# Kernel optimization log

Measured on AMD Instinct MI355X. Metric: run time of the kernel, lower is better.

## Reference

```python
import jax, jax.numpy as jnp
import numpy as np

NUM_HEADS = 16
D_ATT = 64


def setup_inputs() -> dict:
    key = jax.random.key(0)
    ks = jax.random.split(key, 7)
    b, n, hd = 4, 2048, NUM_HEADS * 64  # input last dim = num_heads * per-head embed_dim
    Q_vec = jax.random.normal(ks[0], (b, n, hd), dtype=jnp.float32)
    K_vec = jax.random.normal(ks[1], (b, n, hd), dtype=jnp.float32)
    V_vec = jax.random.normal(ks[2], (b, n, hd), dtype=jnp.float32)
    # torch Linear weights: [out_features, in_features] = [d_attention, per_head_dim]
    W_Q = jax.random.normal(ks[3], (D_ATT, 64), dtype=jnp.float32) * 0.02
    W_K = jax.random.normal(ks[4], (D_ATT, 64), dtype=jnp.float32) * 0.02
    W_V = jax.random.normal(ks[5], (D_ATT, 64), dtype=jnp.float32) * 0.02
    mask = jax.random.bernoulli(ks[6], p=0.9, shape=(b, n))  # bool [b, n]
    return {"Q_vec": Q_vec, "K_vec": K_vec, "V_vec": V_vec,
            "W_Q": W_Q, "W_K": W_K, "W_V": W_V, "mask": mask}


def reference(Q_vec, K_vec, V_vec, W_Q, W_K, W_V, mask):
    b, n, _ = Q_vec.shape
    h = NUM_HEADS
    scaling = 1.0 / np.sqrt(D_ATT).astype(np.float32)

    def split_heads(x):  # b n (h d) -> b h n d
        return x.reshape(b, n, h, -1).transpose(0, 2, 1, 3)

    # Linear applied per-head (weights are [out, in]; y = x @ W^T)
    q = split_heads(Q_vec) @ W_Q.T  # [b,h,n,D_ATT]
    k = split_heads(K_vec) @ W_K.T
    v = split_heads(V_vec) @ W_V.T

    dots = jnp.einsum('bhid,bhjd->bhij', q, k) * scaling  # [b,h,n,n]
    pair_mask = mask[:, None, :] & mask[:, :, None]       # [b,n,n]
    mask_value = -jnp.finfo(dots.dtype).max
    dots = jnp.where(pair_mask[:, None, :, :], dots, mask_value)
    attn = jax.nn.softmax(dots, axis=-1)
    out = jnp.einsum('bhij,bhjd->bhid', attn, v)          # [b,h,n,D_ATT]
    return out.transpose(0, 2, 1, 3).reshape(b, n, h * D_ATT)
```

## Files before the change

### kernel.cpp

```cpp
#include <hip/hip_runtime.h>

#define B_  4
#define N_  2048
#define H_  16
#define HD_ 1024

typedef short  bf16x8 __attribute__((ext_vector_type(8)));
typedef float  f32x4  __attribute__((ext_vector_type(4)));

static __device__ __forceinline__ unsigned short f2bf(float f) {
    unsigned int u = __builtin_bit_cast(unsigned int, f);
    u += 0x7FFFu + ((u >> 16) & 1u);
    return (unsigned short)(u >> 16);
}

__global__ __launch_bounds__(256) void proj_kernel(
    const float* __restrict__ Qv, const float* __restrict__ Kv,
    const float* __restrict__ Vv, const float* __restrict__ WQ,
    const float* __restrict__ WK, const float* __restrict__ WV,
    unsigned short* __restrict__ qs, unsigned short* __restrict__ ks,
    unsigned short* __restrict__ vt)
{
    __shared__ __align__(16) unsigned short xb[64][72];
    __shared__ __align__(16) unsigned short Wb[64][72];
    __shared__ __align__(16) unsigned short sb[64][72];

    const int tid  = threadIdx.x;
    const int wq   = tid >> 6;
    const int lane = tid & 63;
    const int l15  = lane & 15;
    const int quad = lane >> 4;

    const int i0 = blockIdx.x * 64;
    const int h  = blockIdx.y;
    const int b  = blockIdx.z;

    const size_t inbase = ((size_t)b * N_ + i0) * HD_ + h * 64;
    const size_t bh     = (size_t)b * H_ + h;

    #pragma unroll
    for (int p = 0; p < 3; ++p) {
        const float* W   = (p == 0) ? WQ : (p == 1) ? WK : WV;
        const float* inp = ((p == 0) ? Qv : (p == 1) ? Kv : Vv) + inbase;

        __syncthreads();
        for (int v = tid; v < 1024; v += 256) {
            int tok = v >> 4, c4 = (v & 15) * 4;
            float4 f = *reinterpret_cast<const float4*>(inp + (size_t)tok * HD_ + c4);
            uint2 u;
            u.x = f2bf(f.x) | ((unsigned)f2bf(f.y) << 16);
            u.y = f2bf(f.z) | ((unsigned)f2bf(f.w) << 16);
            *reinterpret_cast<uint2*>(&xb[tok][c4]) = u;
            float4 g = *reinterpret_cast<const float4*>(W + (size_t)v * 4);
            uint2 w2;
            w2.x = f2bf(g.x) | ((unsigned)f2bf(g.y) << 16);
            w2.y = f2bf(g.z) | ((unsigned)f2bf(g.w) << 16);
            *reinterpret_cast<uint2*>(&Wb[v >> 4][c4]) = w2;
        }
        __syncthreads();

        bf16x8 ax[2];
        #pragma unroll
        for (int kh = 0; kh < 2; ++kh)
            ax[kh] = *reinterpret_cast<const bf16x8*>(&xb[wq * 16 + l15][kh * 32 + quad * 8]);

        f32x4 C[4];
        #pragma unroll
        for (int t = 0; t < 4; ++t) {
            C[t] = f32x4{0.f, 0.f, 0.f, 0.f};
            #pragma unroll
            for (int kh = 0; kh < 2; ++kh) {
                bf16x8 bw = *reinterpret_cast<const bf16x8*>(&Wb[t * 16 + l15][kh * 32 + quad * 8]);
                C[t] = __builtin_amdgcn_mfma_f32_16x16x32_bf16(ax[kh], bw, C[t], 0, 0, 0);
            }
        }

        if (p < 2) {
            const float scl = (p == 0) ? 0.125f : 1.f;
            #pragma unroll
            for (int t = 0; t < 4; ++t)
                #pragma unroll
                for (int r = 0; r < 4; ++r)
                    sb[wq * 16 + quad * 4 + r][t * 16 + l15] = f2bf(C[t][r] * scl);
            __syncthreads();
            unsigned short* dst = ((p == 0) ? qs : ks) + ((size_t)bh * N_ + i0) * 64;
            for (int v = tid; v < 512; v += 256) {
                int row = v >> 3, c0 = (v & 7) * 8;
                *reinterpret_cast<uint4*>(dst + (size_t)row * 64 + c0) =
                    *reinterpret_cast<const uint4*>(&sb[row][c0]);
            }
        } else {
            #pragma unroll
            for (int t = 0; t < 4; ++t)
                #pragma unroll
                for (int r = 0; r < 4; ++r)
                    sb[t * 16 + l15][wq * 16 + quad * 4 + r] = f2bf(C[t][r]);
            __syncthreads();
            unsigned short* vdst = vt + (size_t)bh * 64 * N_ + i0;
            for (int v = tid; v < 512; v += 256) {
                int d = v >> 3, c0 = (v & 7) * 8;
                *reinterpret_cast<uint4*>(vdst + (size_t)d * N_ + c0) =
                    *reinterpret_cast<const uint4*>(&sb[d][c0]);
            }
        }
    }
}

__global__ __launch_bounds__(256) void attn_kernel(
    const unsigned short* __restrict__ qs, const unsigned short* __restrict__ ks,
    const unsigned short* __restrict__ vt, const int* __restrict__ maskp,
    float* __restrict__ out)
{
    __shared__ __align__(16) unsigned short Ks[64][72];
    __shared__ __align__(16) unsigned short Vt[64][72];
    __shared__ __align__(16) unsigned short Ps[4][16][72];
    __shared__ float kb[64];

    const int tid  = threadIdx.x;
    const int wq   = tid >> 6;
    const int lane = tid & 63;
    const int l15  = lane & 15;
    const int quad = lane >> 4;

    const int i0 = blockIdx.x * 64;
    const int bh = blockIdx.y;
    const int b  = bh >> 4;
    const int h  = bh & 15;

    const unsigned short* qrow = qs + ((size_t)bh * N_ + i0 + wq * 16 + l15) * 64;
    bf16x8 aq[2];
    aq[0] = *reinterpret_cast<const bf16x8*>(qrow + quad * 8);
    aq[1] = *reinterpret_cast<const bf16x8*>(qrow + 32 + quad * 8);

    float qm[4];
    #pragma unroll
    for (int r = 0; r < 4; ++r)
        qm[r] = maskp[b * N_ + i0 + wq * 16 + quad * 4 + r] ? 1.f : 0.f;

    bf16x8 bones;
    {
        short onev = (l15 == 0) ? (short)0x3F80 : (short)0;
        #pragma unroll
        for (int j = 0; j < 8; ++j) bones[j] = onev;
    }

    f32x4 O[4];
    f32x4 L = f32x4{0.f, 0.f, 0.f, 0.f};
    #pragma unroll
    for (int t = 0; t < 4; ++t) O[t] = f32x4{0.f, 0.f, 0.f, 0.f};

    const unsigned short* kbase = ks + (size_t)bh * N_ * 64;
    const unsigned short* vbase = vt + (size_t)bh * 64 * N_;

    for (int kv0 = 0; kv0 < N_; kv0 += 64) {
        __syncthreads();
        #pragma unroll
        for (int it = 0; it < 2; ++it) {
            int r  = (tid >> 3) + it * 32;
            int c0 = (tid & 7) * 8;
            *reinterpret_cast<uint4*>(&Ks[r][c0]) =
                *reinterpret_cast<const uint4*>(kbase + (size_t)(kv0 + r) * 64 + c0);
            *reinterpret_cast<uint4*>(&Vt[r][c0]) =
                *reinterpret_cast<const uint4*>(vbase + (size_t)r * N_ + kv0 + c0);
        }
        if (tid < 64) kb[tid] = maskp[b * N_ + kv0 + tid] ? 0.f : -1e30f;
        __syncthreads();

        f32x4 S[4];
        #pragma unroll
        for (int t = 0; t < 4; ++t) {
            S[t] = f32x4{0.f, 0.f, 0.f, 0.f};
            #pragma unroll
            for (int kh = 0; kh < 2; ++kh) {
                bf16x8 bk = *reinterpret_cast<const bf16x8*>(&Ks[t * 16 + l15][kh * 32 + quad * 8]);
                S[t] = __builtin_amdgcn_mfma_f32_16x16x32_bf16(aq[kh], bk, S[t], 0, 0, 0);
            }
        }

        float kbl[4];
        #pragma unroll
        for (int t = 0; t < 4; ++t) kbl[t] = kb[t * 16 + l15];

        #pragma unroll
        for (int t = 0; t < 4; ++t)
            #pragma unroll
            for (int r = 0; r < 4; ++r) {
                float s = (qm[r] != 0.f) ? (S[t][r] + kbl[t]) : 0.f;
                Ps[wq][quad * 4 + r][t * 16 + l15] = f2bf(__expf(s));
            }

        __builtin_amdgcn_s_waitcnt(0xC07F);

        bf16x8 ap[2];
        #pragma unroll
        for (int kh = 0; kh < 2; ++kh)
            ap[kh] = *reinterpret_cast<const bf16x8*>(&Ps[wq][l15][kh * 32 + quad * 8]);

        #pragma unroll
        for (int t = 0; t < 4; ++t) {
            #pragma unroll
            for (int kh = 0; kh < 2; ++kh) {
                bf16x8 bv = *reinterpret_cast<const bf16x8*>(&Vt[t * 16 + l15][kh * 32 + quad * 8]);
                O[t] = __builtin_amdgcn_mfma_f32_16x16x32_bf16(ap[kh], bv, O[t], 0, 0, 0);
            }
        }
        #pragma unroll
        for (int kh = 0; kh < 2; ++kh)
            L = __builtin_amdgcn_mfma_f32_16x16x32_bf16(ap[kh], bones, L, 0, 0, 0);
    }

    float invl[4];
    #pragma unroll
    for (int r = 0; r < 4; ++r) {
        float l = __shfl(L[r], lane & 48);
        invl[r] = 1.f / l;
    }
    #pragma unroll
    for (int t = 0; t < 4; ++t)
        #pragma unroll
        for (int r = 0; r < 4; ++r) {
            int i = i0 + wq * 16 + quad * 4 + r;
            out[((size_t)b * N_ + i) * HD_ + h * 64 + t * 16 + l15] = O[t][r] * invl[r];
        }
}

extern "C" void kernel_launch(void* const* d_in, const int* in_sizes, int n_in,
                              void* d_out, int out_size, void* d_ws, size_t ws_size,
                              hipStream_t stream)
{
    const float* Qv  = (const float*)d_in[0];
    const float* Kv  = (const float*)d_in[1];
    const float* Vv  = (const float*)d_in[2];
    const float* WQ  = (const float*)d_in[3];
    const float* WK  = (const float*)d_in[4];
    const float* WV  = (const float*)d_in[5];
    const int*   msk = (const int*)d_in[6];
    float* out = (float*)d_out;

    const size_t per = (size_t)B_ * H_ * N_ * 64;
    unsigned short* qsb = (unsigned short*)d_ws;
    unsigned short* ksb = qsb + per;
    unsigned short* vtb = ksb + per;

    proj_kernel<<<dim3(N_ / 64, H_, B_), 256, 0, stream>>>(Qv, Kv, Vv, WQ, WK, WV, qsb, ksb, vtb);
    attn_kernel<<<dim3(N_ / 64, B_ * H_), 256, 0, stream>>>(qsb, ksb, vtb, msk, out);
}
```

Baseline: 279.7 us.

## Split projection per Q/K/V block, fold log2e into exp2, swizzle K/V tile loads

The projection kernel now launches three times as many blocks, each handling one of Q, K or V rather than looping over all three. This raises parallelism and removes the barriers between the three passes. bf16 packing uses a byte-permute of two rounded values, and the V transpose write is vectorised. The attention kernel folds log2(e) into the Q scale so it can call exp2f, replaces the mask select with a multiply, and staggers the rows each thread loads for the K/V tiles to spread memory and LDS bank traffic.

```diff
diff --git a/kernel.cpp b/kernel.cpp
--- a/kernel.cpp
+++ b/kernel.cpp
@@ -12,6 +12,14 @@
     unsigned int u = __builtin_bit_cast(unsigned int, f);
     u += 0x7FFFu + ((u >> 16) & 1u);
     return (unsigned short)(u >> 16);
+}
+
+static __device__ __forceinline__ unsigned rne_hi(float f) {
+    unsigned u = __builtin_bit_cast(unsigned, f);
+    return u + 0x7FFFu + ((u >> 16) & 1u);
+}
+static __device__ __forceinline__ unsigned f2bf2pack(float lo, float hi) {
+    return __builtin_amdgcn_perm(rne_hi(hi), rne_hi(lo), 0x07060302u);
 }
 
 __global__ __launch_bounds__(256) void proj_kernel(
@@ -33,75 +41,75 @@
 
     const int i0 = blockIdx.x * 64;
     const int h  = blockIdx.y;
-    const int b  = blockIdx.z;
+    const int bz = blockIdx.z;
+    const int b  = bz / 3;
+    const int p  = bz - b * 3;
 
     const size_t inbase = ((size_t)b * N_ + i0) * HD_ + h * 64;
     const size_t bh     = (size_t)b * H_ + h;
 
-    #pragma unroll
-    for (int p = 0; p < 3; ++p) {
-        const float* W   = (p == 0) ? WQ : (p == 1) ? WK : WV;
-        const float* inp = ((p == 0) ? Qv : (p == 1) ? Kv : Vv) + inbase;
-
-        __syncthreads();
-        for (int v = tid; v < 1024; v += 256) {
-            int tok = v >> 4, c4 = (v & 15) * 4;
-            float4 f = *reinterpret_cast<const float4*>(inp + (size_t)tok * HD_ + c4);
+    const float* W   = (p == 0) ? WQ : (p == 1) ? WK : WV;
+    const float* inp = ((p == 0) ? Qv : (p == 1) ? Kv : Vv) + inbase;
+
+    for (int v = tid; v < 1024; v += 256) {
+        int tok = v >> 4, c4 = (v & 15) * 4;
+        float4 f = *reinterpret_cast<const float4*>(inp + (size_t)tok * HD_ + c4);
+        uint2 u;
+        u.x = f2bf2pack(f.x, f.y);
+        u.y = f2bf2pack(f.z, f.w);
+        *reinterpret_cast<uint2*>(&xb[tok][c4]) = u;
+        float4 g = *reinterpret_cast<const float4*>(W + (size_t)v * 4);
+        uint2 w2;
+        w2.x = f2bf2pack(g.x, g.y);
+        w2.y = f2bf2pack(g.z, g.w);
+        *reinterpret_cast<uint2*>(&Wb[tok][c4]) = w2;
+    }
+    __syncthreads();
+
+    bf16x8 ax[2];
+    #pragma unroll
+    for (int kh = 0; kh < 2; ++kh)
+        ax[kh] = *reinterpret_cast<const bf16x8*>(&xb[wq * 16 + l15][kh * 32 + quad * 8]);
+
+    f32x4 C[4];
+    #pragma unroll
+    for (int t = 0; t < 4; ++t) {
+        C[t] = f32x4{0.f, 0.f, 0.f, 0.f};
+        #pragma unroll
+        for (int kh = 0; kh < 2; ++kh) {
+            bf16x8 bw = *reinterpret_cast<const bf16x8*>(&Wb[t * 16 + l15][kh * 32 + quad * 8]);
+            C[t] = __builtin_amdgcn_mfma_f32_16x16x32_bf16(ax[kh], bw, C[t], 0, 0, 0);
+        }
+    }
+
+    if (p < 2) {
+        const float scl = (p == 0) ? 0.180336880f : 1.f;
+        #pragma unroll
+        for (int t = 0; t < 4; ++t)
+            #pragma unroll
+            for (int r = 0; r < 4; ++r)
+                sb[wq * 16 + quad * 4 + r][t * 16 + l15] = f2bf(C[t][r] * scl);
+        __syncthreads();
+        unsigned short* dst = ((p == 0) ? qs : ks) + ((size_t)bh * N_ + i0) * 64;
+        for (int v = tid; v < 512; v += 256) {
+            int row = v >> 3, c0 = (v & 7) * 8;
+            *reinterpret_cast<uint4*>(dst + (size_t)row * 64 + c0) =
+                *reinterpret_cast<const uint4*>(&sb[row][c0]);
+        }
+    } else {
+        #pragma unroll
+        for (int t = 0; t < 4; ++t) {
             uint2 u;
-            u.x = f2bf(f.x) | ((unsigned)f2bf(f.y) << 16);
-            u.y = f2bf(f.z) | ((unsigned)f2bf(f.w) << 16);
-            *reinterpret_cast<uint2*>(&xb[tok][c4]) = u;
-            float4 g = *reinterpret_cast<const float4*>(W + (size_t)v * 4);
-            uint2 w2;
-            w2.x = f2bf(g.x) | ((unsigned)f2bf(g.y) << 16);
-            w2.y = f2bf(g.z) | ((unsigned)f2bf(g.w) << 16);
-            *reinterpret_cast<uint2*>(&Wb[v >> 4][c4]) = w2;
-        }
-        __syncthreads();
-
-        bf16x8 ax[2];
-        #pragma unroll
-        for (int kh = 0; kh < 2; ++kh)
-            ax[kh] = *reinterpret_cast<const bf16x8*>(&xb[wq * 16 + l15][kh * 32 + quad * 8]);
-
-        f32x4 C[4];
-        #pragma unroll
-        for (int t = 0; t < 4; ++t) {
-            C[t] = f32x4{0.f, 0.f, 0.f, 0.f};
-            #pragma unroll
-            for (int kh = 0; kh < 2; ++kh) {
-                bf16x8 bw = *reinterpret_cast<const bf16x8*>(&Wb[t * 16 + l15][kh * 32 + quad * 8]);
-                C[t] = __builtin_amdgcn_mfma_f32_16x16x32_bf16(ax[kh], bw, C[t], 0, 0, 0);
-            }
-        }
-
-        if (p < 2) {
-            const float scl = (p == 0) ? 0.125f : 1.f;
-            #pragma unroll
-            for (int t = 0; t < 4; ++t)
-                #pragma unroll
-                for (int r = 0; r < 4; ++r)
-                    sb[wq * 16 + quad * 4 + r][t * 16 + l15] = f2bf(C[t][r] * scl);
-            __syncthreads();
-            unsigned short* dst = ((p == 0) ? qs : ks) + ((size_t)bh * N_ + i0) * 64;
-            for (int v = tid; v < 512; v += 256) {
-                int row = v >> 3, c0 = (v & 7) * 8;
-                *reinterpret_cast<uint4*>(dst + (size_t)row * 64 + c0) =
-                    *reinterpret_cast<const uint4*>(&sb[row][c0]);
-            }
-        } else {
-            #pragma unroll
-            for (int t = 0; t < 4; ++t)
-                #pragma unroll
-                for (int r = 0; r < 4; ++r)
-                    sb[t * 16 + l15][wq * 16 + quad * 4 + r] = f2bf(C[t][r]);
-            __syncthreads();
-            unsigned short* vdst = vt + (size_t)bh * 64 * N_ + i0;
-            for (int v = tid; v < 512; v += 256) {
-                int d = v >> 3, c0 = (v & 7) * 8;
-                *reinterpret_cast<uint4*>(vdst + (size_t)d * N_ + c0) =
-                    *reinterpret_cast<const uint4*>(&sb[d][c0]);
-            }
+            u.x = f2bf2pack(C[t][0], C[t][1]);
+            u.y = f2bf2pack(C[t][2], C[t][3]);
+            *reinterpret_cast<uint2*>(&sb[t * 16 + l15][wq * 16 + quad * 4]) = u;
+        }
+        __syncthreads();
+        unsigned short* vdst = vt + (size_t)bh * 64 * N_ + i0;
+        for (int v = tid; v < 512; v += 256) {
+            int d = v >> 3, c0 = (v & 7) * 8;
+            *reinterpret_cast<uint4*>(vdst + (size_t)d * N_ + c0) =
+                *reinterpret_cast<const uint4*>(&sb[d][c0]);
         }
     }
 }
@@ -127,6 +135,10 @@
     const int b  = bh >> 4;
     const int h  = bh & 15;
 
+    const int sg  = tid & 7;
+    const int rsw = ((tid >> 3) & 24) | (((tid >> 3) & 7) ^ sg);
+    const int c0s = sg * 8;
+
     const unsigned short* qrow = qs + ((size_t)bh * N_ + i0 + wq * 16 + l15) * 64;
     bf16x8 aq[2];
     aq[0] = *reinterpret_cast<const bf16x8*>(qrow + quad * 8);
@@ -156,12 +168,11 @@
         __syncthreads();
         #pragma unroll
         for (int it = 0; it < 2; ++it) {
-            int r  = (tid >> 3) + it * 32;
-            int c0 = (tid & 7) * 8;
-            *reinterpret_cast<uint4*>(&Ks[r][c0]) =
-                *reinterpret_cast<const uint4*>(kbase + (size_t)(kv0 + r) * 64 + c0);
-            *reinterpret_cast<uint4*>(&Vt[r][c0]) =
-                *reinterpret_cast<const uint4*>(vbase + (size_t)r * N_ + kv0 + c0);
+            int r = rsw + it * 32;
+            *reinterpret_cast<uint4*>(&Ks[r][c0s]) =
+                *reinterpret_cast<const uint4*>(kbase + (size_t)(kv0 + r) * 64 + c0s);
+            *reinterpret_cast<uint4*>(&Vt[r][c0s]) =
+                *reinterpret_cast<const uint4*>(vbase + (size_t)r * N_ + kv0 + c0s);
         }
         if (tid < 64) kb[tid] = maskp[b * N_ + kv0 + tid] ? 0.f : -1e30f;
         __syncthreads();
@@ -185,8 +196,8 @@
         for (int t = 0; t < 4; ++t)
             #pragma unroll
             for (int r = 0; r < 4; ++r) {
-                float s = (qm[r] != 0.f) ? (S[t][r] + kbl[t]) : 0.f;
-                Ps[wq][quad * 4 + r][t * 16 + l15] = f2bf(__expf(s));
+                float s = (S[t][r] + kbl[t]) * qm[r];
+                Ps[wq][quad * 4 + r][t * 16 + l15] = f2bf(exp2f(s));
             }
 
         __builtin_amdgcn_s_waitcnt(0xC07F);
@@ -242,6 +253,6 @@
     unsigned short* ksb = qsb + per;
     unsigned short* vtb = ksb + per;
 
-    proj_kernel<<<dim3(N_ / 64, H_, B_), 256, 0, stream>>>(Qv, Kv, Vv, WQ, WK, WV, qsb, ksb, vtb);
+    proj_kernel<<<dim3(N_ / 64, H_, B_ * 3), 256, 0, stream>>>(Qv, Kv, Vv, WQ, WK, WV, qsb, ksb, vtb);
     attn_kernel<<<dim3(N_ / 64, B_ * H_), 256, 0, stream>>>(qsb, ksb, vtb, msk, out);
 }
```

New measurement: 327.5 us. 17.1% more time.
